# Performance work log

Measured on AMD Instinct MI355X. Metric: run time of the kernel, lower is better.

Reference implementation:

```python
import jax, jax.numpy as jnp
import numpy as np

SPLIT_K = 64  # cfg.split_k; bilinear feature dim d = W_dim // SPLIT_K


def _per_doc(seq, att, ep, W_s, W_o, W_c, A_bl, b_bl, W_attn, v_attn, clf_W, clf_b):
    # seq [S,H], att [heads,S,S], ep [N,M] mention token positions
    # entity rep: logsumexp pooling over mention embeddings
    rep = jax.scipy.special.logsumexp(seq[ep], axis=1)                 # [N,H]
    # entity attention: sum of mention attention rows
    ga = att[:, ep, :].sum(axis=2).transpose(1, 0, 2)                  # [N,heads,S]
    # pairwise localized context: product of head-wise attentions, summed over heads
    pa = jnp.einsum('ihs,jhs->ijs', ga, ga)                            # [N,N,S]
    pa = pa / pa.sum(-1, keepdims=True)
    ctx = jnp.einsum('ijs,sh->ijh', pa, seq) @ W_c                     # [N,N,W]
    Zs = jnp.tanh((rep @ W_s)[:, None, :] + ctx)                       # [N,N,W]
    Zo = jnp.tanh((rep @ W_o)[:, None, :] + ctx)
    N, Wd = Zs.shape[0], Zs.shape[-1]
    d = Wd // SPLIT_K
    # torch: split into Wd//SPLIT_K chunks of size SPLIT_K, stack at -1 -> [N,N,SPLIT_K,d]
    Zs4 = Zs.reshape(N, N, d, SPLIT_K).swapaxes(-1, -2)
    Zo4 = Zo.reshape(N, N, d, SPLIT_K).swapaxes(-1, -2)
    # grouped bilinear scoring, summed over the SPLIT_K groups (bias added per group)
    g = jnp.einsum('ijkp,opq,ijkq->ijo', Zs4, A_bl, Zo4) + SPLIT_K * b_bl  # [N,N,W]
    # axis attention over the N x N pair grid: row-wise and column-wise softmax contexts
    e = jnp.tanh(g @ W_attn) @ v_attn                                  # [N,N]
    a_row = jax.nn.softmax(e, axis=1)
    a_col = jax.nn.softmax(e, axis=0)
    r = (g
         + jnp.einsum('ij,ijd->id', a_row, g)[:, None, :]
         + jnp.einsum('ij,ijd->jd', a_col, g)[None, :, :])
    return r @ clf_W + clf_b                                           # [N,N,num_class]


def setup_inputs() -> dict:
    key = jax.random.key(0)
    ks = jax.random.split(key, 12)
    B, S, H, Hh, N, M = 4, 1024, 768, 12, 32, 4
    Wd, AD, C = 768, 256, 97
    d = Wd // SPLIT_K
    p = lambda k, shape: jax.random.normal(k, shape, dtype=jnp.float32) * 0.02
    return {
        'sequence_output': jax.random.normal(ks[0], (B, S, H), dtype=jnp.float32),
        'attention': jax.random.uniform(ks[1], (B, Hh, S, S), dtype=jnp.float32),
        'entity_pos': jax.random.randint(ks[2], (B, N, M), 0, S),
        'W_s': p(ks[3], (H, Wd)),
        'W_o': p(ks[4], (H, Wd)),
        'W_c': p(ks[5], (H, Wd)),
        'A_bl': p(ks[6], (Wd, d, d)),
        'b_bl': p(ks[7], (Wd,)),
        'W_attn': p(ks[8], (Wd, AD)),
        'v_attn': p(ks[9], (AD,)),
        'clf_W': p(ks[10], (Wd, C)),
        'clf_b': p(ks[11], (C,)),
    }


def reference(sequence_output, attention, entity_pos, W_s, W_o, W_c, A_bl, b_bl,
              W_attn, v_attn, clf_W, clf_b):
    f = jax.vmap(_per_doc, in_axes=(0, 0, 0) + (None,) * 9)
    return f(sequence_output, attention, entity_pos, W_s, W_o, W_c, A_bl, b_bl,
             W_attn, v_attn, clf_W, clf_b)  # [B,N,N,num_class]
```

## Files before the change

### kernel.cpp

```cpp
#include <hip/hip_runtime.h>
#include <hip/hip_bf16.h>
#include <math.h>

#define BB 4
#define SS 1024
#define HH 768
#define NHEAD 12
#define NN 32
#define MM 4
#define WD 768
#define AD 256
#define NC 97
#define SPK 64
#define DD 12
#define KP 160

typedef __attribute__((ext_vector_type(8))) short short8;
typedef __attribute__((ext_vector_type(4))) float float4_t;

__device__ inline unsigned short f2bf(float x) {
  union { float f; unsigned int u; } v; v.f = x;
  unsigned int r = v.u + 0x7fffu + ((v.u >> 16) & 1u);
  return (unsigned short)(r >> 16);
}
__device__ inline float bf2f(unsigned short x) {
  union { unsigned int u; float f; } v; v.u = ((unsigned int)x) << 16;
  return v.f;
}

__device__ __forceinline__ void gl_lds16(unsigned short* l, const unsigned short* g) {
  __builtin_amdgcn_global_load_lds(
      (const __attribute__((address_space(1))) unsigned int*)g,
      (__attribute__((address_space(3))) unsigned int*)l, 16, 0, 0);
}

__device__ __forceinline__ void transpose_tile(const float* __restrict__ in,
                                               unsigned short* __restrict__ out,
                                               int R, int C, int Cp, int t, int tilesR) {
  __shared__ float tile[32][33];
  int r0 = (t % tilesR) * 32, c0 = (t / tilesR) * 32;
  int tx = threadIdx.x & 31, ty = threadIdx.x >> 5;
#pragma unroll
  for (int i = 0; i < 32; i += 8) {
    int r = r0 + ty + i, c = c0 + tx;
    tile[ty + i][tx] = (c < C) ? in[(size_t)r * C + c] : 0.f;
  }
  __syncthreads();
#pragma unroll
  for (int i = 0; i < 32; i += 8) {
    int c = c0 + ty + i, r = r0 + tx;
    if (c < Cp) out[(size_t)c * R + r] = f2bf(tile[tx][ty + i]);
  }
}

__global__ __launch_bounds__(256) void k_prep(
    const float* __restrict__ seq, const float* __restrict__ W_c,
    const float* __restrict__ W_attn, const float* __restrict__ clf_W,
    const float* __restrict__ W_s, const float* __restrict__ W_o,
    const float* __restrict__ A_bl,
    unsigned short* __restrict__ seqB, unsigned short* __restrict__ WcT,
    unsigned short* __restrict__ WaT, unsigned short* __restrict__ clfT,
    unsigned short* __restrict__ WsoT, unsigned short* __restrict__ AblB) {
  int bid = blockIdx.x;
  if (bid < 3072) {
    int i = (bid * 256 + threadIdx.x) * 4;
    float4 v = *(const float4*)&seq[i];
    seqB[i + 0] = f2bf(v.x); seqB[i + 1] = f2bf(v.y);
    seqB[i + 2] = f2bf(v.z); seqB[i + 3] = f2bf(v.w);
    return;
  }
  bid -= 3072;
  if (bid < 576) { transpose_tile(W_c, WcT, HH, WD, WD, bid, 24); return; }
  bid -= 576;
  if (bid < 192) { transpose_tile(W_attn, WaT, WD, AD, AD, bid, 24); return; }
  bid -= 192;
  if (bid < 96)  { transpose_tile(clf_W, clfT, WD, NC, 128, bid, 24); return; }
  bid -= 96;
  if (bid < 576) { transpose_tile(W_s, WsoT, HH, WD, WD, bid, 24); return; }
  bid -= 576;
  if (bid < 576) { transpose_tile(W_o, WsoT + (size_t)WD * HH, HH, WD, WD, bid, 24); return; }
  bid -= 576;
  {
    int idx = bid * 256 + threadIdx.x;
    int w = idx / KP, pq = idx % KP;
    if (w < WD) AblB[idx] = (pq < DD * DD) ? f2bf(A_bl[(size_t)w * DD * DD + pq]) : 0;
  }
}

__global__ void k_rep(const float* __restrict__ seq, const int* __restrict__ ep,
                      unsigned short* __restrict__ repB) {
  int bn = blockIdx.x; int b = bn / NN;
  const int* e = ep + (size_t)bn * MM;
  int i0 = e[0], i1 = e[1], i2 = e[2], i3 = e[3];
  const float* sb = seq + (size_t)b * SS * HH;
  for (int h = threadIdx.x; h < HH; h += blockDim.x) {
    float v0 = sb[(size_t)i0 * HH + h];
    float v1 = sb[(size_t)i1 * HH + h];
    float v2 = sb[(size_t)i2 * HH + h];
    float v3 = sb[(size_t)i3 * HH + h];
    float mx = fmaxf(fmaxf(v0, v1), fmaxf(v2, v3));
    float s = expf(v0 - mx) + expf(v1 - mx) + expf(v2 - mx) + expf(v3 - mx);
    repB[(size_t)bn * HH + h] = f2bf(mx + logf(s));
  }
}

__global__ void k_ga(const float* __restrict__ att, const int* __restrict__ ep,
                     float* __restrict__ ga) {
  int t = blockIdx.x;
  int h = t % NHEAD;
  int bn = t / NHEAD;
  int b = bn / NN;
  const int* e = ep + (size_t)bn * MM;
  int i0 = e[0], i1 = e[1], i2 = e[2], i3 = e[3];
  const float* ab = att + ((size_t)b * NHEAD + h) * SS * SS;
  float* go = ga + ((size_t)bn * NHEAD + h) * SS;
  for (int s = threadIdx.x; s < SS; s += blockDim.x) {
    go[s] = ab[(size_t)i0 * SS + s] + ab[(size_t)i1 * SS + s] +
            ab[(size_t)i2 * SS + s] + ab[(size_t)i3 * SS + s];
  }
}

__global__ __launch_bounds__(256) void k_pa(const float* __restrict__ ga,
                                            unsigned short* __restrict__ pa) {
  int t = blockIdx.x;
  int j = t % NN;
  int i = (t / NN) % NN;
  int b = t / (NN * NN);
  const float* gi = ga + ((size_t)(b * NN + i)) * NHEAD * SS;
  const float* gj = ga + ((size_t)(b * NN + j)) * NHEAD * SS;
  float acc[4];
  float tot = 0.f;
#pragma unroll
  for (int r = 0; r < 4; ++r) {
    int s = threadIdx.x + r * 256;
    float a = 0.f;
#pragma unroll
    for (int h = 0; h < NHEAD; ++h) a += gi[h * SS + s] * gj[h * SS + s];
    acc[r] = a;
    tot += a;
  }
  __shared__ float red[256];
  red[threadIdx.x] = tot;
  __syncthreads();
  for (int o = 128; o > 0; o >>= 1) {
    if (threadIdx.x < o) red[threadIdx.x] += red[threadIdx.x + o];
    __syncthreads();
  }
  float inv = 1.0f / red[0];
  unsigned short* po = pa + (size_t)t * SS;
#pragma unroll
  for (int r = 0; r < 4; ++r) {
    int s = threadIdx.x + r * 256;
    po[s] = f2bf(acc[r] * inv);
  }
}

template <int MODE>
__global__ __launch_bounds__(256)
void k_mm(const unsigned short* __restrict__ A, const unsigned short* __restrict__ B,
          void* __restrict__ Cv, int Nc, int K, int ldb, int ldc,
          long long sA, long long sB, long long sC,
          const float* __restrict__ bias, float biasScale,
          const float* __restrict__ rcWp, const float* __restrict__ clf_b) {
  A += (long long)blockIdx.z * sA;
  B += (long long)blockIdx.z * sB;
  __shared__ __align__(16) unsigned short As[128 * 32];
  __shared__ __align__(16) unsigned short Bs[128 * 32];
  const int tid = threadIdx.x;
  const int m0 = blockIdx.y * 128;
  const int n0 = blockIdx.x * 128;
  const int lane = tid & 63;
  const int w = tid >> 6;
  const int wr = (w >> 1) * 64, wc = (w & 1) * 64;
  const int q = lane >> 4, l16 = lane & 15;
  const int lr = lane >> 2, lq = lane & 3;
  float4_t acc[4][4] = {};
  const unsigned short* Ag0 = A + (size_t)(m0 + w * 16 + lr) * K + lq * 8;
  const unsigned short* Ag1 = Ag0 + (size_t)64 * K;
  const unsigned short* Bg0 = B + (size_t)(n0 + w * 16 + lr) * ldb + lq * 8;
  const unsigned short* Bg1 = Bg0 + (size_t)64 * ldb;
  unsigned short* Al0 = &As[(w * 16) * 32];
  unsigned short* Al1 = &As[(64 + w * 16) * 32];
  unsigned short* Bl0 = &Bs[(w * 16) * 32];
  unsigned short* Bl1 = &Bs[(64 + w * 16) * 32];
  for (int k0 = 0; k0 < K; k0 += 32) {
    gl_lds16(Al0, Ag0 + k0);
    gl_lds16(Al1, Ag1 + k0);
    gl_lds16(Bl0, Bg0 + k0);
    gl_lds16(Bl1, Bg1 + k0);
    __syncthreads();
    short8 af[4], bfr[4];
#pragma unroll
    for (int i = 0; i < 4; ++i)
      af[i] = *(const short8*)&As[(wr + i * 16 + l16) * 32 + q * 8];
#pragma unroll
    for (int j = 0; j < 4; ++j)
      bfr[j] = *(const short8*)&Bs[(wc + j * 16 + l16) * 32 + q * 8];
#pragma unroll
    for (int i = 0; i < 4; ++i)
#pragma unroll
      for (int j = 0; j < 4; ++j)
        acc[i][j] = __builtin_amdgcn_mfma_f32_16x16x32_bf16(af[i], bfr[j], acc[i][j], 0, 0, 0);
    __syncthreads();
  }
  float* Cf = (float*)Cv + (long long)blockIdx.z * sC;
  unsigned short* Cb = (unsigned short*)Cv + (long long)blockIdx.z * sC;
#pragma unroll
  for (int i = 0; i < 4; ++i) {
    int mbase = m0 + wr + i * 16 + q * 4;
#pragma unroll
    for (int j = 0; j < 4; ++j) {
      int n = n0 + wc + j * 16 + l16;
      if (n < Nc) {
        float badd = bias ? biasScale * bias[n] : 0.f;
#pragma unroll
        for (int r = 0; r < 4; ++r) {
          int m = mbase + r;
          float v = acc[i][j][r] + badd;
          if (MODE == 3) {
            int b = m >> 10, ii = (m >> 5) & 31, jj = m & 31;
            v += rcWp[(size_t)(b * NN + ii) * NC + n] +
                 rcWp[(size_t)(BB * NN + b * NN + jj) * NC + n] + clf_b[n];
          }
          if (MODE == 1)      Cb[(size_t)m * ldc + n] = f2bf(v);
          else if (MODE == 2) Cf[(size_t)n * ldc + m] = v;
          else                Cf[(size_t)m * ldc + n] = v;
        }
      }
    }
  }
}

__global__ __launch_bounds__(256) void k_M(const unsigned short* __restrict__ ctx,
                                           const float* __restrict__ rso,
                                           unsigned short* __restrict__ Mm) {
  int t = blockIdx.x;
  const float* rsi = rso + (size_t)(t >> 5) * 1536;
  __shared__ float zsT[64 * 13];
  __shared__ float zoT[64 * 13];
  const unsigned short* cx = ctx + (size_t)t * WD;
  for (int wd = threadIdx.x; wd < WD; wd += blockDim.x) {
    float c = bf2f(cx[wd]);
    int k = wd & 63, p = wd >> 6;
    zsT[k * 13 + p] = tanhf(rsi[wd] + c);
    zoT[k * 13 + p] = tanhf(rsi[WD + wd] + c);
  }
  __syncthreads();
  int pq = threadIdx.x;
  if (pq < KP) {
    float s = 0.f;
    if (pq < DD * DD) {
      int p = pq / DD, qq = pq % DD;
#pragma unroll
      for (int k = 0; k < SPK; ++k) s += zsT[k * 13 + p] * zoT[k * 13 + qq];
    }
    Mm[(size_t)t * KP + pq] = f2bf(s);
  }
}

__global__ __launch_bounds__(AD) void k_e(const float* __restrict__ tbuf,
                                          const float* __restrict__ v_attn,
                                          float* __restrict__ e) {
  int r = blockIdx.x;
  int a = threadIdx.x;
  float v = tanhf(tbuf[(size_t)r * AD + a]) * v_attn[a];
  __shared__ float red[AD];
  red[a] = v;
  __syncthreads();
  for (int o = AD / 2; o > 0; o >>= 1) {
    if (a < o) red[a] += red[a + o];
    __syncthreads();
  }
  if (a == 0) e[r] = red[0];
}

__global__ __launch_bounds__(1024) void k_softmax(const float* __restrict__ e,
                                                  float* __restrict__ arow,
                                                  float* __restrict__ acol) {
  int b = blockIdx.x;
  __shared__ float E[NN][NN + 1];
  __shared__ float Rm[NN], Rs[NN];
  int tid = threadIdx.x;
  int i = tid / NN, j = tid % NN;
  E[i][j] = e[(size_t)b * NN * NN + tid];
  __syncthreads();
  if (tid < NN) {
    float mx = -1e30f;
    for (int jj = 0; jj < NN; ++jj) mx = fmaxf(mx, E[tid][jj]);
    float s = 0.f;
    for (int jj = 0; jj < NN; ++jj) s += expf(E[tid][jj] - mx);
    Rm[tid] = mx;
    Rs[tid] = s;
  }
  __syncthreads();
  arow[(size_t)b * NN * NN + tid] = expf(E[i][j] - Rm[i]) / Rs[i];
  __syncthreads();
  if (tid < NN) {
    float mx = -1e30f;
    for (int ii = 0; ii < NN; ++ii) mx = fmaxf(mx, E[ii][tid]);
    float s = 0.f;
    for (int ii = 0; ii < NN; ++ii) s += expf(E[ii][tid] - mx);
    Rm[tid] = mx;
    Rs[tid] = s;
  }
  __syncthreads();
  acol[(size_t)b * NN * NN + tid] = expf(E[i][j] - Rm[j]) / Rs[j];
}

__global__ __launch_bounds__(256) void k_rowcol(const unsigned short* __restrict__ g,
                                                const float* __restrict__ arow,
                                                const float* __restrict__ acol,
                                                unsigned short* __restrict__ rc) {
  int t = blockIdx.x;
  int which = t / (BB * NN);
  int bn = t % (BB * NN);
  int b = bn / NN, x = bn % NN;
  const unsigned short* gb = g + (size_t)b * NN * NN * WD;
  unsigned short* out = rc + ((size_t)which * BB * NN + bn) * WD;
  for (int o = threadIdx.x; o < WD; o += blockDim.x) {
    float s = 0.f;
    if (which == 0) {
      const float* ar = arow + (size_t)b * NN * NN + (size_t)x * NN;
#pragma unroll 4
      for (int jj = 0; jj < NN; ++jj)
        s += ar[jj] * bf2f(gb[((size_t)x * NN + jj) * WD + o]);
    } else {
      const float* ac = acol + (size_t)b * NN * NN;
#pragma unroll 4
      for (int ii = 0; ii < NN; ++ii)
        s += ac[(size_t)ii * NN + x] * bf2f(gb[((size_t)ii * NN + x) * WD + o]);
    }
    out[o] = f2bf(s);
  }
}

extern "C" void kernel_launch(void* const* d_in, const int* in_sizes, int n_in,
                              void* d_out, int out_size, void* d_ws, size_t ws_size,
                              hipStream_t stream) {
  const float* seq    = (const float*)d_in[0];
  const float* att    = (const float*)d_in[1];
  const int*   ep     = (const int*)d_in[2];
  const float* W_s    = (const float*)d_in[3];
  const float* W_o    = (const float*)d_in[4];
  const float* W_c    = (const float*)d_in[5];
  const float* A_bl   = (const float*)d_in[6];
  const float* b_bl   = (const float*)d_in[7];
  const float* W_attn = (const float*)d_in[8];
  const float* v_attn = (const float*)d_in[9];
  const float* clf_W  = (const float*)d_in[10];
  const float* clf_b  = (const float*)d_in[11];
  float* out = (float*)d_out;

  char* base = (char*)d_ws;
  size_t off = 0;
  auto alloc = [&](size_t bytes) {
    char* p = base + off;
    off += (bytes + 255) & ~(size_t)255;
    return p;
  };
  unsigned short* repB = (unsigned short*)alloc((size_t)BB * NN * HH * 2);
  float* rso  = (float*)alloc((size_t)BB * NN * 2 * WD * 4);
  float* ga   = (float*)alloc((size_t)BB * NN * NHEAD * SS * 4);
  unsigned short* paB  = (unsigned short*)alloc((size_t)BB * NN * NN * SS * 2);
  unsigned short* seqB = (unsigned short*)alloc((size_t)BB * SS * HH * 2);
  unsigned short* WcT  = (unsigned short*)alloc((size_t)HH * WD * 2);
  unsigned short* WaT  = (unsigned short*)alloc((size_t)AD * WD * 2);
  unsigned short* clfT = (unsigned short*)alloc((size_t)128 * WD * 2);
  unsigned short* WsoT = (unsigned short*)alloc((size_t)2 * WD * HH * 2);
  unsigned short* scT  = (unsigned short*)alloc((size_t)WD * BB * SS * 2);
  unsigned short* ctxB = (unsigned short*)alloc((size_t)BB * NN * NN * WD * 2);
  unsigned short* MmB  = (unsigned short*)alloc((size_t)BB * NN * NN * KP * 2);
  unsigned short* AblB = (unsigned short*)alloc((size_t)WD * KP * 2);
  float* ebuf = (float*)alloc((size_t)BB * NN * NN * 4);
  float* arow = (float*)alloc((size_t)BB * NN * NN * 4);
  float* acol = (float*)alloc((size_t)BB * NN * NN * 4);
  unsigned short* rcB = (unsigned short*)alloc((size_t)2 * BB * NN * WD * 2);
  float* rcW  = (float*)alloc((size_t)2 * BB * NN * NC * 4);
  float* tbuf = ga;
  unsigned short* gB = paB;

  const float* nof = nullptr;

  k_prep<<<dim3(5568), dim3(256), 0, stream>>>(seq, W_c, W_attn, clf_W, W_s, W_o,
                                               A_bl, seqB, WcT, WaT, clfT, WsoT, AblB);

  k_rep<<<dim3(BB * NN), dim3(256), 0, stream>>>(seq, ep, repB);
  k_ga<<<dim3(BB * NN * NHEAD), dim3(256), 0, stream>>>(att, ep, ga);

  k_mm<2><<<dim3(1, 12, 1), dim3(256), 0, stream>>>(
      WsoT, repB, rso, BB * NN, HH, HH, 2 * WD, 0LL, 0LL, 0LL, nof, 0.f, nof, nof);

  k_mm<1><<<dim3(BB * SS / 128, WD / 128, 1), dim3(256), 0, stream>>>(
      WcT, seqB, scT, BB * SS, HH, HH, BB * SS, 0LL, 0LL, 0LL, nof, 0.f, nof, nof);

  k_pa<<<dim3(BB * NN * NN), dim3(256), 0, stream>>>(ga, paB);

  k_mm<1><<<dim3(WD / 128, NN * NN / 128, BB), dim3(256), 0, stream>>>(
      paB, scT, ctxB, WD, SS, BB * SS, WD,
      (long long)NN * NN * SS, (long long)SS, (long long)NN * NN * WD,
      nof, 0.f, nof, nof);

  k_M<<<dim3(BB * NN * NN), dim3(256), 0, stream>>>(ctxB, rso, MmB);

  k_mm<1><<<dim3(WD / 128, BB * NN * NN / 128, 1), dim3(256), 0, stream>>>(
      MmB, AblB, gB, WD, KP, KP, WD, 0LL, 0LL, 0LL, b_bl, (float)SPK, nof, nof);

  k_mm<0><<<dim3(AD / 128, BB * NN * NN / 128, 1), dim3(256), 0, stream>>>(
      gB, WaT, tbuf, AD, WD, WD, AD, 0LL, 0LL, 0LL, nof, 0.f, nof, nof);

  k_e<<<dim3(BB * NN * NN), dim3(AD), 0, stream>>>(tbuf, v_attn, ebuf);

  k_softmax<<<dim3(BB), dim3(NN * NN), 0, stream>>>(ebuf, arow, acol);

  k_rowcol<<<dim3(2 * BB * NN), dim3(256), 0, stream>>>(gB, arow, acol, rcB);

  k_mm<0><<<dim3(1, 2, 1), dim3(256), 0, stream>>>(
      rcB, clfT, rcW, NC, WD, WD, NC, 0LL, 0LL, 0LL, nof, 0.f, nof, nof);

  k_mm<3><<<dim3(1, BB * NN * NN / 128, 1), dim3(256), 0, stream>>>(
      gB, clfT, out, NC, WD, WD, NC, 0LL, 0LL, 0LL, nof, 0.f, rcW, clf_b);
}
```

Baseline: 468.7 us.

## Fold W_attn into bilinear weights, fuse front kernels and softmax-rowcol-classifier

Precomputes F = A_bl·W_attn and the bias term so the attention logits e come straight from the small-K MmB GEMM, with tanh, v_attn dot and reduction fused into the GEMM epilogue via atomics. This removes the g·W_attn GEMM and the k_e pass. It also merges the ga, rep and prep kernels into one front launch, stores ga in bf16 with vectorised loads in k_pa, and folds softmax, row/col context and the clf projection into a single k_rowcolW kernel. The cost is the serial precompute of F inside the front kernel, bf16 rounding of ga, and atomic accumulation order in e.

Measured after the change: 468.8 us. No clear change (+0.0%).

```diff
diff --git a/kernel.cpp b/kernel.cpp
--- a/kernel.cpp
+++ b/kernel.cpp
@@ -16,6 +16,7 @@
 #define KP 160
 
 typedef __attribute__((ext_vector_type(8))) short short8;
+typedef __attribute__((ext_vector_type(4))) short sshort4;
 typedef __attribute__((ext_vector_type(4))) float float4_t;
 
 __device__ inline unsigned short f2bf(float x) {
@@ -53,17 +54,66 @@
   }
 }
 
-__global__ __launch_bounds__(256) void k_prep(
-    const float* __restrict__ seq, const float* __restrict__ W_c,
-    const float* __restrict__ W_attn, const float* __restrict__ clf_W,
+__global__ __launch_bounds__(256) void k_front(
+    const float* __restrict__ seq, const float* __restrict__ att,
+    const int* __restrict__ ep, const float* __restrict__ W_c,
     const float* __restrict__ W_s, const float* __restrict__ W_o,
-    const float* __restrict__ A_bl,
+    const float* __restrict__ clf_W, const float* __restrict__ A_bl,
+    const float* __restrict__ W_attn, const float* __restrict__ b_bl,
+    unsigned short* __restrict__ gaB, unsigned short* __restrict__ FB,
+    float* __restrict__ tb, float* __restrict__ ebuf,
     unsigned short* __restrict__ seqB, unsigned short* __restrict__ WcT,
-    unsigned short* __restrict__ WaT, unsigned short* __restrict__ clfT,
-    unsigned short* __restrict__ WsoT, unsigned short* __restrict__ AblB) {
+    unsigned short* __restrict__ WsoT, unsigned short* __restrict__ clfT,
+    unsigned short* __restrict__ AblB, unsigned short* __restrict__ repB) {
   int bid = blockIdx.x;
+  int tid = threadIdx.x;
+  if (bid < 1536) {
+    int h = bid % NHEAD;
+    int bn = bid / NHEAD;
+    int b = bn / NN;
+    const int* e = ep + (size_t)bn * MM;
+    int i0 = e[0], i1 = e[1], i2 = e[2], i3 = e[3];
+    const float* ab = att + ((size_t)b * NHEAD + h) * SS * SS;
+    unsigned short* go = gaB + ((size_t)bn * NHEAD + h) * SS;
+#pragma unroll
+    for (int r = 0; r < 4; ++r) {
+      int s = tid + r * 256;
+      go[s] = f2bf(ab[(size_t)i0 * SS + s] + ab[(size_t)i1 * SS + s] +
+                   ab[(size_t)i2 * SS + s] + ab[(size_t)i3 * SS + s]);
+    }
+    return;
+  }
+  bid -= 1536;
+  if (bid < 256) {
+    int a = bid;
+    int k = tid;
+    if (k < KP) {
+      float acc = 0.f;
+      if (k < DD * DD) {
+        for (int w = 0; w < WD; ++w)
+          acc += A_bl[(size_t)w * (DD * DD) + k] * W_attn[(size_t)w * AD + a];
+      }
+      FB[(size_t)a * KP + k] = f2bf(acc);
+    }
+    return;
+  }
+  bid -= 256;
+  if (bid < 1) {
+    int a = tid;
+    float acc = 0.f;
+    for (int w = 0; w < WD; ++w) acc += b_bl[w] * W_attn[(size_t)w * AD + a];
+    tb[a] = (float)SPK * acc;
+    return;
+  }
+  bid -= 1;
+  if (bid < 16) {
+    int idx = bid * 256 + tid;
+    if (idx < BB * NN * NN) ebuf[idx] = 0.f;
+    return;
+  }
+  bid -= 16;
   if (bid < 3072) {
-    int i = (bid * 256 + threadIdx.x) * 4;
+    int i = (bid * 256 + tid) * 4;
     float4 v = *(const float4*)&seq[i];
     seqB[i + 0] = f2bf(v.x); seqB[i + 1] = f2bf(v.y);
     seqB[i + 2] = f2bf(v.z); seqB[i + 3] = f2bf(v.w);
@@ -72,73 +122,55 @@
   bid -= 3072;
   if (bid < 576) { transpose_tile(W_c, WcT, HH, WD, WD, bid, 24); return; }
   bid -= 576;
-  if (bid < 192) { transpose_tile(W_attn, WaT, WD, AD, AD, bid, 24); return; }
-  bid -= 192;
-  if (bid < 96)  { transpose_tile(clf_W, clfT, WD, NC, 128, bid, 24); return; }
-  bid -= 96;
   if (bid < 576) { transpose_tile(W_s, WsoT, HH, WD, WD, bid, 24); return; }
   bid -= 576;
   if (bid < 576) { transpose_tile(W_o, WsoT + (size_t)WD * HH, HH, WD, WD, bid, 24); return; }
   bid -= 576;
+  if (bid < 96)  { transpose_tile(clf_W, clfT, WD, NC, 128, bid, 24); return; }
+  bid -= 96;
+  if (bid < 480) {
+    int idx = bid * 256 + tid;
+    int w = idx / KP, pq = idx % KP;
+    AblB[idx] = (pq < DD * DD) ? f2bf(A_bl[(size_t)w * DD * DD + pq]) : 0;
+    return;
+  }
+  bid -= 480;
   {
-    int idx = bid * 256 + threadIdx.x;
-    int w = idx / KP, pq = idx % KP;
-    if (w < WD) AblB[idx] = (pq < DD * DD) ? f2bf(A_bl[(size_t)w * DD * DD + pq]) : 0;
-  }
-}
-
-__global__ void k_rep(const float* __restrict__ seq, const int* __restrict__ ep,
-                      unsigned short* __restrict__ repB) {
-  int bn = blockIdx.x; int b = bn / NN;
-  const int* e = ep + (size_t)bn * MM;
-  int i0 = e[0], i1 = e[1], i2 = e[2], i3 = e[3];
-  const float* sb = seq + (size_t)b * SS * HH;
-  for (int h = threadIdx.x; h < HH; h += blockDim.x) {
-    float v0 = sb[(size_t)i0 * HH + h];
-    float v1 = sb[(size_t)i1 * HH + h];
-    float v2 = sb[(size_t)i2 * HH + h];
-    float v3 = sb[(size_t)i3 * HH + h];
-    float mx = fmaxf(fmaxf(v0, v1), fmaxf(v2, v3));
-    float s = expf(v0 - mx) + expf(v1 - mx) + expf(v2 - mx) + expf(v3 - mx);
-    repB[(size_t)bn * HH + h] = f2bf(mx + logf(s));
-  }
-}
-
-__global__ void k_ga(const float* __restrict__ att, const int* __restrict__ ep,
-                     float* __restrict__ ga) {
-  int t = blockIdx.x;
-  int h = t % NHEAD;
-  int bn = t / NHEAD;
-  int b = bn / NN;
-  const int* e = ep + (size_t)bn * MM;
-  int i0 = e[0], i1 = e[1], i2 = e[2], i3 = e[3];
-  const float* ab = att + ((size_t)b * NHEAD + h) * SS * SS;
-  float* go = ga + ((size_t)bn * NHEAD + h) * SS;
-  for (int s = threadIdx.x; s < SS; s += blockDim.x) {
-    go[s] = ab[(size_t)i0 * SS + s] + ab[(size_t)i1 * SS + s] +
-            ab[(size_t)i2 * SS + s] + ab[(size_t)i3 * SS + s];
-  }
-}
-
-__global__ __launch_bounds__(256) void k_pa(const float* __restrict__ ga,
+    int bn = bid; int b = bn / NN;
+    const int* e = ep + (size_t)bn * MM;
+    int i0 = e[0], i1 = e[1], i2 = e[2], i3 = e[3];
+    const float* sb = seq + (size_t)b * SS * HH;
+    for (int h = tid; h < HH; h += 256) {
+      float v0 = sb[(size_t)i0 * HH + h];
+      float v1 = sb[(size_t)i1 * HH + h];
+      float v2 = sb[(size_t)i2 * HH + h];
+      float v3 = sb[(size_t)i3 * HH + h];
+      float mx = fmaxf(fmaxf(v0, v1), fmaxf(v2, v3));
+      float s = expf(v0 - mx) + expf(v1 - mx) + expf(v2 - mx) + expf(v3 - mx);
+      repB[(size_t)bn * HH + h] = f2bf(mx + logf(s));
+    }
+  }
+}
+
+__global__ __launch_bounds__(256) void k_pa(const unsigned short* __restrict__ gaB,
                                             unsigned short* __restrict__ pa) {
   int t = blockIdx.x;
   int j = t % NN;
   int i = (t / NN) % NN;
   int b = t / (NN * NN);
-  const float* gi = ga + ((size_t)(b * NN + i)) * NHEAD * SS;
-  const float* gj = ga + ((size_t)(b * NN + j)) * NHEAD * SS;
-  float acc[4];
-  float tot = 0.f;
-#pragma unroll
-  for (int r = 0; r < 4; ++r) {
-    int s = threadIdx.x + r * 256;
-    float a = 0.f;
-#pragma unroll
-    for (int h = 0; h < NHEAD; ++h) a += gi[h * SS + s] * gj[h * SS + s];
-    acc[r] = a;
-    tot += a;
-  }
+  const unsigned short* gi = gaB + ((size_t)(b * NN + i)) * NHEAD * SS;
+  const unsigned short* gj = gaB + ((size_t)(b * NN + j)) * NHEAD * SS;
+  int s0 = threadIdx.x * 4;
+  float acc[4] = {0.f, 0.f, 0.f, 0.f};
+#pragma unroll
+  for (int h = 0; h < NHEAD; ++h) {
+    sshort4 a4 = *(const sshort4*)&gi[h * SS + s0];
+    sshort4 b4 = *(const sshort4*)&gj[h * SS + s0];
+#pragma unroll
+    for (int r = 0; r < 4; ++r)
+      acc[r] += bf2f((unsigned short)a4[r]) * bf2f((unsigned short)b4[r]);
+  }
+  float tot = acc[0] + acc[1] + acc[2] + acc[3];
   __shared__ float red[256];
   red[threadIdx.x] = tot;
   __syncthreads();
@@ -147,12 +179,10 @@
     __syncthreads();
   }
   float inv = 1.0f / red[0];
-  unsigned short* po = pa + (size_t)t * SS;
-#pragma unroll
-  for (int r = 0; r < 4; ++r) {
-    int s = threadIdx.x + r * 256;
-    po[s] = f2bf(acc[r] * inv);
-  }
+  unsigned short ov[4];
+#pragma unroll
+  for (int r = 0; r < 4; ++r) ov[r] = f2bf(acc[r] * inv);
+  *(sshort4*)&pa[(size_t)t * SS + s0] = *(sshort4*)ov;
 }
 
 template <int MODE>
@@ -203,6 +233,26 @@
         acc[i][j] = __builtin_amdgcn_mfma_f32_16x16x32_bf16(af[i], bfr[j], acc[i][j], 0, 0, 0);
     __syncthreads();
   }
+  if (MODE == 4) {
+    float* ep = (float*)Cv;
+#pragma unroll
+    for (int i = 0; i < 4; ++i) {
+#pragma unroll
+      for (int r = 0; r < 4; ++r) {
+        float part = 0.f;
+#pragma unroll
+        for (int j = 0; j < 4; ++j) {
+          int n = n0 + wc + j * 16 + l16;
+          float v = acc[i][j][r] + bias[n];
+          part += tanhf(v) * rcWp[n];
+        }
+#pragma unroll
+        for (int d = 1; d < 16; d <<= 1) part += __shfl_xor(part, d, 16);
+        if (l16 == 0) atomicAdd(&ep[m0 + wr + i * 16 + q * 4 + r], part);
+      }
+    }
+    return;
+  }
   float* Cf = (float*)Cv + (long long)blockIdx.z * sC;
   unsigned short* Cb = (unsigned short*)Cv + (long long)blockIdx.z * sC;
 #pragma unroll
@@ -258,79 +308,44 @@
   }
 }
 
-__global__ __launch_bounds__(AD) void k_e(const float* __restrict__ tbuf,
-                                          const float* __restrict__ v_attn,
-                                          float* __restrict__ e) {
-  int r = blockIdx.x;
-  int a = threadIdx.x;
-  float v = tanhf(tbuf[(size_t)r * AD + a]) * v_attn[a];
-  __shared__ float red[AD];
-  red[a] = v;
+__global__ __launch_bounds__(256) void k_rowcolW(const float* __restrict__ e,
+                                                 const unsigned short* __restrict__ g,
+                                                 const float* __restrict__ clf_W,
+                                                 float* __restrict__ rcW) {
+  int t = blockIdx.x;
+  int which = t >> 7;
+  int bn = t & 127;
+  int b = bn >> 5, x = bn & 31;
+  int tid = threadIdx.x;
+  __shared__ float av[NN];
+  __shared__ float rcs[WD];
+  if (tid < NN)
+    av[tid] = (which == 0) ? e[(size_t)b * 1024 + x * NN + tid]
+                           : e[(size_t)b * 1024 + tid * NN + x];
   __syncthreads();
-  for (int o = AD / 2; o > 0; o >>= 1) {
-    if (a < o) red[a] += red[a + o];
-    __syncthreads();
-  }
-  if (a == 0) e[r] = red[0];
-}
-
-__global__ __launch_bounds__(1024) void k_softmax(const float* __restrict__ e,
-                                                  float* __restrict__ arow,
-                                                  float* __restrict__ acol) {
-  int b = blockIdx.x;
-  __shared__ float E[NN][NN + 1];
-  __shared__ float Rm[NN], Rs[NN];
-  int tid = threadIdx.x;
-  int i = tid / NN, j = tid % NN;
-  E[i][j] = e[(size_t)b * NN * NN + tid];
+  float mx = -1e30f;
+#pragma unroll 8
+  for (int k = 0; k < NN; ++k) mx = fmaxf(mx, av[k]);
+  float sm = 0.f;
+  float wk[NN];
+#pragma unroll 8
+  for (int k = 0; k < NN; ++k) { wk[k] = expf(av[k] - mx); sm += wk[k]; }
+  float inv = 1.0f / sm;
+  const unsigned short* gb = g + (size_t)b * 1024 * WD;
+  for (int o = tid; o < WD; o += 256) {
+    float s = 0.f;
+#pragma unroll 8
+    for (int k = 0; k < NN; ++k) {
+      int pair = (which == 0) ? x * NN + k : k * NN + x;
+      s += wk[k] * bf2f(gb[(size_t)pair * WD + o]);
+    }
+    rcs[o] = s * inv;
+  }
   __syncthreads();
-  if (tid < NN) {
-    float mx = -1e30f;
-    for (int jj = 0; jj < NN; ++jj) mx = fmaxf(mx, E[tid][jj]);
+  if (tid < NC) {
     float s = 0.f;
-    for (int jj = 0; jj < NN; ++jj) s += expf(E[tid][jj] - mx);
-    Rm[tid] = mx;
-    Rs[tid] = s;
-  }
-  __syncthreads();
-  arow[(size_t)b * NN * NN + tid] = expf(E[i][j] - Rm[i]) / Rs[i];
-  __syncthreads();
-  if (tid < NN) {
-    float mx = -1e30f;
-    for (int ii = 0; ii < NN; ++ii) mx = fmaxf(mx, E[ii][tid]);
-    float s = 0.f;
-    for (int ii = 0; ii < NN; ++ii) s += expf(E[ii][tid] - mx);
-    Rm[tid] = mx;
-    Rs[tid] = s;
-  }
-  __syncthreads();
-  acol[(size_t)b * NN * NN + tid] = expf(E[i][j] - Rm[j]) / Rs[j];
-}
-
-__global__ __launch_bounds__(256) void k_rowcol(const unsigned short* __restrict__ g,
-                                                const float* __restrict__ arow,
-                                                const float* __restrict__ acol,
-                                                unsigned short* __restrict__ rc) {
-  int t = blockIdx.x;
-  int which = t / (BB * NN);
-  int bn = t % (BB * NN);
-  int b = bn / NN, x = bn % NN;
-  const unsigned short* gb = g + (size_t)b * NN * NN * WD;
-  unsigned short* out = rc + ((size_t)which * BB * NN + bn) * WD;
-  for (int o = threadIdx.x; o < WD; o += blockDim.x) {
-    float s = 0.f;
-    if (which == 0) {
-      const float* ar = arow + (size_t)b * NN * NN + (size_t)x * NN;
-#pragma unroll 4
-      for (int jj = 0; jj < NN; ++jj)
-        s += ar[jj] * bf2f(gb[((size_t)x * NN + jj) * WD + o]);
-    } else {
-      const float* ac = acol + (size_t)b * NN * NN;
-#pragma unroll 4
-      for (int ii = 0; ii < NN; ++ii)
-        s += ac[(size_t)ii * NN + x] * bf2f(gb[((size_t)ii * NN + x) * WD + o]);
-    }
-    out[o] = f2bf(s);
+    for (int o = 0; o < WD; ++o) s += rcs[o] * clf_W[(size_t)o * NC + tid];
+    rcW[(size_t)(which * 128 + bn) * NC + tid] = s;
   }
 }
 
@@ -360,40 +375,35 @@
   };
   unsigned short* repB = (unsigned short*)alloc((size_t)BB * NN * HH * 2);
   float* rso  = (float*)alloc((size_t)BB * NN * 2 * WD * 4);
-  float* ga   = (float*)alloc((size_t)BB * NN * NHEAD * SS * 4);
+  unsigned short* gaB  = (unsigned short*)alloc((size_t)BB * NN * NHEAD * SS * 2);
   unsigned short* paB  = (unsigned short*)alloc((size_t)BB * NN * NN * SS * 2);
   unsigned short* seqB = (unsigned short*)alloc((size_t)BB * SS * HH * 2);
   unsigned short* WcT  = (unsigned short*)alloc((size_t)HH * WD * 2);
-  unsigned short* WaT  = (unsigned short*)alloc((size_t)AD * WD * 2);
   unsigned short* clfT = (unsigned short*)alloc((size_t)128 * WD * 2);
   unsigned short* WsoT = (unsigned short*)alloc((size_t)2 * WD * HH * 2);
   unsigned short* scT  = (unsigned short*)alloc((size_t)WD * BB * SS * 2);
   unsigned short* ctxB = (unsigned short*)alloc((size_t)BB * NN * NN * WD * 2);
   unsigned short* MmB  = (unsigned short*)alloc((size_t)BB * NN * NN * KP * 2);
   unsigned short* AblB = (unsigned short*)alloc((size_t)WD * KP * 2);
+  unsigned short* FB   = (unsigned short*)alloc((size_t)AD * KP * 2);
+  float* tb   = (float*)alloc((size_t)AD * 4);
   float* ebuf = (float*)alloc((size_t)BB * NN * NN * 4);
-  float* arow = (float*)alloc((size_t)BB * NN * NN * 4);
-  float* acol = (float*)alloc((size_t)BB * NN * NN * 4);
-  unsigned short* rcB = (unsigned short*)alloc((size_t)2 * BB * NN * WD * 2);
   float* rcW  = (float*)alloc((size_t)2 * BB * NN * NC * 4);
-  float* tbuf = ga;
   unsigned short* gB = paB;
 
   const float* nof = nullptr;
 
-  k_prep<<<dim3(5568), dim3(256), 0, stream>>>(seq, W_c, W_attn, clf_W, W_s, W_o,
-                                               A_bl, seqB, WcT, WaT, clfT, WsoT, AblB);
-
-  k_rep<<<dim3(BB * NN), dim3(256), 0, stream>>>(seq, ep, repB);
-  k_ga<<<dim3(BB * NN * NHEAD), dim3(256), 0, stream>>>(att, ep, ga);
+  k_front<<<dim3(7313), dim3(256), 0, stream>>>(
+      seq, att, ep, W_c, W_s, W_o, clf_W, A_bl, W_attn, b_bl,
+      gaB, FB, tb, ebuf, seqB, WcT, WsoT, clfT, AblB, repB);
+
+  k_mm<1><<<dim3(BB * SS / 128, WD / 128, 1), dim3(256), 0, stream>>>(
+      WcT, seqB, scT, BB * SS, HH, HH, BB * SS, 0LL, 0LL, 0LL, nof, 0.f, nof, nof);
 
   k_mm<2><<<dim3(1, 12, 1), dim3(256), 0, stream>>>(
       WsoT, repB, rso, BB * NN, HH, HH, 2 * WD, 0LL, 0LL, 0LL, nof, 0.f, nof, nof);
 
-  k_mm<1><<<dim3(BB * SS / 128, WD / 128, 1), dim3(256), 0, stream>>>(
-      WcT, seqB, scT, BB * SS, HH, HH, BB * SS, 0LL, 0LL, 0LL, nof, 0.f, nof, nof);
-
-  k_pa<<<dim3(BB * NN * NN), dim3(256), 0, stream>>>(ga, paB);
+  k_pa<<<dim3(BB * NN * NN), dim3(256), 0, stream>>>(gaB, paB);
 
   k_mm<1><<<dim3(WD / 128, NN * NN / 128, BB), dim3(256), 0, stream>>>(
       paB, scT, ctxB, WD, SS, BB * SS, WD,
@@ -402,20 +412,13 @@
 
   k_M<<<dim3(BB * NN * NN), dim3(256), 0, stream>>>(ctxB, rso, MmB);
 
+  k_mm<4><<<dim3(AD / 128, BB * NN * NN / 128, 1), dim3(256), 0, stream>>>(
+      MmB, FB, ebuf, AD, KP, KP, 0, 0LL, 0LL, 0LL, tb, 1.f, v_attn, nof);
+
   k_mm<1><<<dim3(WD / 128, BB * NN * NN / 128, 1), dim3(256), 0, stream>>>(
       MmB, AblB, gB, WD, KP, KP, WD, 0LL, 0LL, 0LL, b_bl, (float)SPK, nof, nof);
 
-  k_mm<0><<<dim3(AD / 128, BB * NN * NN / 128, 1), dim3(256), 0, stream>>>(
-      gB, WaT, tbuf, AD, WD, WD, AD, 0LL, 0LL, 0LL, nof, 0.f, nof, nof);
-
-  k_e<<<dim3(BB * NN * NN), dim3(AD), 0, stream>>>(tbuf, v_attn, ebuf);
-
-  k_softmax<<<dim3(BB), dim3(NN * NN), 0, stream>>>(ebuf, arow, acol);
-
-  k_rowcol<<<dim3(2 * BB * NN), dim3(256), 0, stream>>>(gB, arow, acol, rcB);
-
-  k_mm<0><<<dim3(1, 2, 1), dim3(256), 0, stream>>>(
-      rcB, clfT, rcW, NC, WD, WD, NC, 0LL, 0LL, 0LL, nof, 0.f, nof, nof);
+  k_rowcolW<<<dim3(2 * BB * NN), dim3(256), 0, stream>>>(ebuf, gB, clf_W, rcW);
 
   k_mm<3><<<dim3(1, BB * NN * NN / 128, 1), dim3(256), 0, stream>>>(
       gB, clfT, out, NC, WD, WD, NC, 0LL, 0LL, 0LL, nof, 0.f, rcW, clf_b);
```
